# Optimization experiments

Hardware: AMD Instinct MI355X
Metric: run time of the kernel (lower is better)

The kernel has to match this reference:

```python
import jax, jax.numpy as jnp
import numpy as np

B = 32768
PASSES = 4

# mask layout: (batch, digit, row, col), values in {0,1}

def _to_lines(m, d):
    """Reorder so the last axis enumerates the 9 cells of a line and axis -2 the 9 lines."""
    if d == 'h':
        return m                      # lines = rows, cells = cols
    if d == 'v':
        return jnp.swapaxes(m, 2, 3)  # lines = cols, cells = rows
    b = m.shape[0]                    # lines = 3x3 boxes
    return m.reshape(b, 9, 3, 3, 3, 3).transpose(0, 1, 2, 4, 3, 5).reshape(b, 9, 9, 9)

_from_lines = _to_lines  # all three reorderings are self-inverse


def filter_line(m, d):
    """SudokuFilterHVBox: remove a solved cell's digit from all other cells in its line."""
    l = _to_lines(m, d)
    cnt = l.sum(axis=1, keepdims=True)                 # candidates per cell
    solved = l * (cnt == 1).astype(l.dtype)            # one-hot solved cells
    other = solved.sum(axis=-1, keepdims=True) - solved  # same digit solved elsewhere in line
    out = l * (other == 0).astype(l.dtype)
    return _from_lines(out, d)


def unique_line(m, d):
    """SudokuUniqueHVBox (hidden single): if a digit fits only one cell in a line, fix it."""
    l = _to_lines(m, d)
    cnt_line = l.sum(axis=-1, keepdims=True)           # per-digit count in the line
    hidden = l * (cnt_line == 1).astype(l.dtype)       # lone placements
    has = hidden.sum(axis=1, keepdims=True) > 0        # cell hosts a hidden single
    out = jnp.where(has, hidden, l)
    return _from_lines(out, d)


def doubles_line(m, d):
    """SudokuDigitsDoubles (naked pair): two identical 2-candidate cells in a line
    eliminate those digits from the rest of the line."""
    l = _to_lines(m, d)                                # (B, d, line, cell)
    cnt = l.sum(axis=1, keepdims=True)
    pm = l * (cnt == 2).astype(l.dtype)                # patterns of 2-candidate cells
    dot = jnp.einsum('bdlc,bdle->blce', pm, pm)        # pattern overlap between cells
    eye = jnp.eye(9, dtype=l.dtype)
    match = (dot == 2).astype(l.dtype) * (1.0 - eye)   # identical pair at another cell
    pairflag = match.sum(-1) > 0                       # (B, line, cell) part of a naked pair
    pair_digit = pm * pairflag[:, None, :, :].astype(l.dtype)
    total_pd = pair_digit.sum(-1, keepdims=True)       # digit belongs to some pair in line
    remove = (total_pd > 0) & (pair_digit == 0)
    out = l * (1.0 - remove.astype(l.dtype))
    return _from_lines(out, d)


def pointing(m, d):
    """SudokuDigitsInOneLineAtBox: if a digit's box candidates lie in one row/col,
    remove that digit from the rest of the row/col outside the box."""
    b = m.shape[0]
    v = m.reshape(b, 9, 3, 3, 3, 3)                    # (B, d, br, ri, bc, ci)
    if d == 'h':
        pres = v.sum(axis=5) > 0                       # (B,d,br,ri,bc) digit in row of box
        nrows = pres.sum(axis=3, keepdims=True)
        point = pres & (nrows == 1)                    # confined to single row within box
        tot = point.sum(axis=4, keepdims=True)         # over bc
        rem = (tot - point) > 0                        # pointing from another box hits us
        out = v * (1.0 - rem[..., None].astype(v.dtype))
    else:
        pres = v.sum(axis=3) > 0                       # (B,d,br,bc,ci) digit in col of box
        ncols = pres.sum(axis=4, keepdims=True)
        point = pres & (ncols == 1)
        tot = point.sum(axis=2, keepdims=True)         # over br
        rem = (tot - point) > 0
        out = v * (1.0 - rem[:, :, :, None, :, :].astype(v.dtype))
    return out.reshape(b, 9, 9, 9)


def _forward_mask(mask):
    for _ in range(PASSES):
        mask = filter_line(mask, 'box')
        mask = pointing(mask, 'h')
        mask = pointing(mask, 'v')
        mask = unique_line(mask, 'h')
        mask = unique_line(mask, 'v')
        mask = unique_line(mask, 'box')
        mask = doubles_line(mask, 'v')   # original code instantiates doubles_h with 'v'
        mask = doubles_line(mask, 'v')
        mask = doubles_line(mask, 'box')
    return mask


def setup_inputs() -> dict:
    key = jax.random.key(0)
    mask = jax.random.randint(key, (B, 9, 9, 9), 0, 2).astype(jnp.float32)
    return {"mask": mask}


def reference(mask):
    out = _forward_mask(mask)
    cnt = out.sum(axis=1)                              # candidates per cell
    solved = jnp.all(cnt == 1, axis=(1, 2))            # (B,) puzzle fully determined
    return (out, solved)
```

## Files before the change

kernel.cpp:

```cpp
#include <hip/hip_runtime.h>
#include <stdint.h>

#define NB 32768
#define NPASS 4
#define FULL27 0x07FFFFFFu
#define NBF (NB * 729)
#define NWORDS (NBF / 32)
#define PACK_BLKS (NWORDS / 256)
#define PUZ_PER_BLK 64
#define SOLVE_BLKS (NB / PUZ_PER_BLK)
#define BLK_DW 1458


__device__ __forceinline__ uint32_t colfold(uint32_t w) {
    return (w | (w >> 9) | (w >> 18)) & 0x1FFu;
}
__device__ __forceinline__ uint32_t colmaj2(uint32_t w) {
    return ((w & (w >> 9)) | ((w | (w >> 9)) & (w >> 18))) & 0x1FFu;
}
__device__ __forceinline__ uint32_t rotA(uint32_t v) {
    return (uint32_t)__builtin_amdgcn_update_dpp(0, (int)v, 0x09, 0xF, 0xF, true);
}
__device__ __forceinline__ uint32_t rotB(uint32_t v) {
    return (uint32_t)__builtin_amdgcn_update_dpp(0, (int)v, 0x12, 0xF, 0xF, true);
}

__global__ __launch_bounds__(256)
void pack_kernel(const uint32_t* __restrict__ in, uint32_t* __restrict__ ws) {
    const int g = blockIdx.x * 256 + threadIdx.x;
    const uint4* src = (const uint4*)in + (size_t)g * 8;
    uint32_t acc = 0u;
    #pragma unroll
    for (int j = 0; j < 8; ++j) {
        uint4 v = src[j];
        uint32_t n = ((v.x >> 23) & 1u) | (((v.y >> 23) & 1u) << 1)
                   | (((v.z >> 23) & 1u) << 2) | (((v.w >> 23) & 1u) << 3);
        acc |= n << (4 * j);
    }
    ws[g] = acc;
}

__global__ __launch_bounds__(256)
void solve_kernel(const uint32_t* __restrict__ ws, float* __restrict__ out,
                  float* __restrict__ solved) {
    __shared__ uint32_t lds[BLK_DW + 2];
    const int tid = threadIdx.x;
    const int q = tid >> 2;
    const int band = tid & 3;
    const int P0 = blockIdx.x * PUZ_PER_BLK;

    {
        const uint2* wsrc = (const uint2*)(ws + (size_t)blockIdx.x * BLK_DW);
        uint2* ldst = (uint2*)lds;
        #pragma unroll
        for (int i = 0; i < 3; ++i) {
            int j = i * 256 + tid;
            if (j < 729) ldst[j] = wsrc[j];
        }
    }
    __syncthreads();

    uint32_t bd[9];
    {
        const int bb0 = q * 729 + band * 27;
        #pragma unroll
        for (int d = 0; d < 9; ++d) {
            int bit = bb0 + d * 81;
            int di = bit >> 5, sh = bit & 31;
            uint64_t both = (uint64_t)lds[di] | ((uint64_t)lds[di + 1] << 32);
            bd[d] = (uint32_t)(both >> sh) & FULL27;
        }
    }
    __syncthreads();

    #pragma unroll 1
    for (int pass = 0; pass < NPASS; ++pass) {
        {
            uint32_t on = 0, tw = 0, fo = 0;
            #pragma unroll
            for (int d = 0; d < 9; ++d) {
                uint32_t c = on & bd[d];
                on ^= bd[d]; fo |= tw & c; tw ^= c;
            }
            uint32_t ex1 = on & ~tw & ~fo;
            #pragma unroll
            for (int d = 0; d < 9; ++d) {
                uint32_t s = bd[d] & ex1;
                #pragma unroll
                for (int k = 0; k < 3; ++k) {
                    uint32_t bm = 0x1C0E07u << (3 * k);
                    uint32_t sm = s & bm;
                    uint32_t multi = sm & (sm - 1u);
                    uint32_t keep = (sm == 0u) ? 0xFFFFFFFFu : (~bm | (multi ? 0u : sm));
                    bd[d] &= keep;
                }
            }
        }

        #pragma unroll
        for (int d = 0; d < 9; ++d) {
            uint32_t w = bd[d];
            uint32_t t = (w | (w >> 1) | (w >> 2)) & 0x01249249u;
            uint32_t sum = (t & 0x1FFu) + ((t >> 9) & 0x1FFu) + ((t >> 18) & 0x1FFu);
            uint32_t single = sum & ~(sum >> 1) & 0x49u;
            uint32_t point = t & (single * 0x40201u);
            uint32_t clearm = 0;
            #pragma unroll
            for (int r = 0; r < 3; ++r) {
                uint32_t pr = (point >> (9 * r)) & 0x1FFu;
                uint32_t multi = pr & (pr - 1u);
                uint32_t segkeep = multi ? 0u : pr * 7u;
                uint32_t rc = pr ? ((0x1FFu & ~segkeep) << (9 * r)) : 0u;
                clearm |= rc;
            }
            bd[d] = w & ~clearm;
        }

        {
            uint32_t pnt[9];
            #pragma unroll
            for (int d = 0; d < 9; ++d) {
                uint32_t w = bd[d];
                uint32_t qq = colfold(w);
                uint32_t u = (qq & 0x49u) + ((qq >> 1) & 0x49u) + ((qq >> 2) & 0x49u);
                uint32_t single = u & ~(u >> 1) & 0x49u;
                pnt[d] = qq & (single * 7u);
            }
            #pragma unroll
            for (int d = 0; d < 9; ++d) {
                uint32_t o = rotA(pnt[d]) | rotB(pnt[d]);
                bd[d] &= ~(o * 0x40201u);
            }
        }

        {
            uint32_t hid[9], has = 0;
            #pragma unroll
            for (int d = 0; d < 9; ++d) {
                uint32_t w = bd[d], h = 0;
                #pragma unroll
                for (int r = 0; r < 3; ++r) {
                    uint32_t x = w & (0x1FFu << (9 * r));
                    h |= (x & (x - 1u)) ? 0u : x;
                }
                hid[d] = h; has |= h;
            }
            #pragma unroll
            for (int d = 0; d < 9; ++d) bd[d] = (bd[d] & ~has) | hid[d];
        }

        {
            uint32_t hid[9], has = 0;
            #pragma unroll
            for (int d = 0; d < 9; ++d) {
                uint32_t w = bd[d];
                uint32_t q0 = colfold(w), m0 = colmaj2(w);
                uint32_t ex = q0 | (m0 << 9);
                uint32_t ea = rotA(ex);
                uint32_t eb = rotB(ex);
                uint32_t qa = ea & 0x1FFu, ma = ea >> 9;
                uint32_t qb = eb & 0x1FFu, mb = eb >> 9;
                uint32_t ge2 = m0 | ma | mb | (q0 & qa) | (q0 & qb) | (qa & qb);
                uint32_t ex1c = (q0 | qa | qb) & ~ge2;
                hid[d] = w & ((ex1c & q0) * 0x40201u);
                has |= hid[d];
            }
            #pragma unroll
            for (int d = 0; d < 9; ++d) bd[d] = (bd[d] & ~has) | hid[d];
        }

        {
            uint32_t hid[9], has = 0;
            #pragma unroll
            for (int d = 0; d < 9; ++d) {
                uint32_t w = bd[d], h = 0;
                #pragma unroll
                for (int k = 0; k < 3; ++k) {
                    uint32_t x = w & (0x1C0E07u << (3 * k));
                    h |= (x & (x - 1u)) ? 0u : x;
                }
                hid[d] = h; has |= h;
            }
            #pragma unroll
            for (int d = 0; d < 9; ++d) bd[d] = (bd[d] & ~has) | hid[d];
        }

        #pragma unroll 1
        for (int rep = 0; rep < 2; ++rep) {
            uint32_t on = 0, tw = 0, fo = 0;
            #pragma unroll
            for (int d = 0; d < 9; ++d) {
                uint32_t c = on & bd[d];
                on ^= bd[d]; fo |= tw & c; tw ^= c;
            }
            uint32_t ex2 = tw & ~on & ~fo;
            uint32_t Q[9], K[9];
            #pragma unroll
            for (int d = 0; d < 9; ++d) { Q[d] = bd[d] & ex2; K[d] = 0u; }
            #pragma unroll
            for (int d1 = 0; d1 < 9; ++d1)
                #pragma unroll
                for (int d2 = d1 + 1; d2 < 9; ++d2) {
                    uint32_t P = Q[d1] & Q[d2];
                    uint32_t f0 = colfold(P), g0 = colmaj2(P);
                    uint32_t ex = f0 | (g0 << 9);
                    uint32_t ea = rotA(ex);
                    uint32_t eb = rotB(ex);
                    uint32_t fa = ea & 0x1FFu, ga = ea >> 9;
                    uint32_t fb = eb & 0x1FFu, gb = eb >> 9;
                    uint32_t dup = g0 | ga | gb | (f0 & fa) | (f0 & fb) | (fa & fb);
                    uint32_t sK = P & (dup * 0x40201u);
                    K[d1] |= sK; K[d2] |= sK;
                }
            #pragma unroll
            for (int d = 0; d < 9; ++d) {
                uint32_t kc = colfold(K[d]);
                uint32_t cols = kc | rotA(kc) | rotB(kc);
                uint32_t em = cols * 0x40201u;
                bd[d] = (bd[d] & ~em) | K[d];
            }
        }

        {
            uint32_t on = 0, tw = 0, fo = 0;
            #pragma unroll
            for (int d = 0; d < 9; ++d) {
                uint32_t c = on & bd[d];
                on ^= bd[d]; fo |= tw & c; tw ^= c;
            }
            uint32_t ex2 = tw & ~on & ~fo;
            uint32_t Q[9], K[9];
            #pragma unroll
            for (int d = 0; d < 9; ++d) { Q[d] = bd[d] & ex2; K[d] = 0u; }
            #pragma unroll
            for (int d1 = 0; d1 < 9; ++d1)
                #pragma unroll
                for (int d2 = d1 + 1; d2 < 9; ++d2) {
                    uint32_t P = Q[d1] & Q[d2];
                    #pragma unroll
                    for (int k = 0; k < 3; ++k) {
                        uint32_t m = P & (0x1C0E07u << (3 * k));
                        uint32_t s = (m & (m - 1u)) ? m : 0u;
                        K[d1] |= s; K[d2] |= s;
                    }
                }
            #pragma unroll
            for (int d = 0; d < 9; ++d)
                #pragma unroll
                for (int k = 0; k < 3; ++k) {
                    uint32_t bm = 0x1C0E07u << (3 * k);
                    uint32_t t = K[d] & bm;
                    uint32_t mask = t ? (~bm | t) : 0xFFFFFFFFu;
                    bd[d] &= mask;
                }
        }
    }

    {
        uint32_t on = 0, tw = 0, fo = 0;
        #pragma unroll
        for (int d = 0; d < 9; ++d) {
            uint32_t c = on & bd[d];
            on ^= bd[d]; fo |= tw & c; tw ^= c;
        }
        uint32_t okb = ((on & ~tw & ~fo) == FULL27) ? 1u : 0u;
        uint32_t all = okb & rotA(okb) & rotB(okb);
        if (band == 0) solved[P0 + q] = all ? 1.0f : 0.0f;
    }

    for (int j = tid; j < BLK_DW + 2; j += 256) lds[j] = 0u;
    __syncthreads();
    if (band != 3) {
        const int pbit = q * 729;
        #pragma unroll
        for (int d = 0; d < 9; ++d) {
            int bitbase = pbit + d * 81 + band * 27;
            int di = bitbase >> 5;
            int sh = bitbase & 31;
            uint64_t both = (uint64_t)bd[d] << sh;
            atomicOr(&lds[di], (uint32_t)both);
            atomicOr(&lds[di + 1], (uint32_t)(both >> 32));
        }
    }
    __syncthreads();
    {
        float4* dst4 = (float4*)(out + (size_t)P0 * 729);
        #pragma unroll 4
        for (int i = 0; i < 46; ++i) {
            int j = i * 256 + tid;
            if (j < 11664) {
                uint32_t nib = (lds[j >> 3] >> ((j & 7) * 4)) & 0xFu;
                dst4[j] = make_float4((float)(nib & 1u), (float)((nib >> 1) & 1u),
                                      (float)((nib >> 2) & 1u), (float)((nib >> 3) & 1u));
            }
        }
    }
}

extern "C" void kernel_launch(void* const* d_in, const int* in_sizes, int n_in,
                              void* d_out, int out_size, void* d_ws, size_t ws_size,
                              hipStream_t stream) {
    const uint32_t* in = (const uint32_t*)d_in[0];
    float* out = (float*)d_out;
    float* solved = out + (size_t)NB * 729;
    uint32_t* ws = (uint32_t*)d_ws;

    pack_kernel<<<PACK_BLKS, 256, 0, stream>>>(in, ws);
    solve_kernel<<<SOLVE_BLKS, 256, 0, stream>>>(ws, out, solved);
}
```

Measured before the change: 216.2 us.

## Fuse bit-packing into solve kernel using DPP lane combining into LDS

Removes the separate pack kernel and its workspace round trip. Each solve block now reads its own float input slice directly, extracts one bit per float, and combines nibbles across neighbouring lanes with DPP swizzles before writing 16-bit halves into shared memory. This drops one launch and the global write and re-read of the packed workspace. In exchange, the solve kernel gets more load-phase work, clamped redundant loads, and lower per-block occupancy during the pack phase.

Measured after the change: 215.6 us. About the same (-0.3%).

```diff
diff --git a/kernel.cpp b/kernel.cpp
--- a/kernel.cpp
+++ b/kernel.cpp
@@ -4,12 +4,10 @@
 #define NB 32768
 #define NPASS 4
 #define FULL27 0x07FFFFFFu
-#define NBF (NB * 729)
-#define NWORDS (NBF / 32)
-#define PACK_BLKS (NWORDS / 256)
 #define PUZ_PER_BLK 64
 #define SOLVE_BLKS (NB / PUZ_PER_BLK)
 #define BLK_DW 1458
+#define BLK_V4 11664
 
 
 __device__ __forceinline__ uint32_t colfold(uint32_t w) {
@@ -24,38 +22,47 @@
 __device__ __forceinline__ uint32_t rotB(uint32_t v) {
     return (uint32_t)__builtin_amdgcn_update_dpp(0, (int)v, 0x12, 0xF, 0xF, true);
 }
+__device__ __forceinline__ uint32_t dppx1(uint32_t v) {
+    return (uint32_t)__builtin_amdgcn_update_dpp(0, (int)v, 0xB1, 0xF, 0xF, true);
+}
+__device__ __forceinline__ uint32_t dppx2(uint32_t v) {
+    return (uint32_t)__builtin_amdgcn_update_dpp(0, (int)v, 0x4E, 0xF, 0xF, true);
+}
 
 __global__ __launch_bounds__(256)
-void pack_kernel(const uint32_t* __restrict__ in, uint32_t* __restrict__ ws) {
-    const int g = blockIdx.x * 256 + threadIdx.x;
-    const uint4* src = (const uint4*)in + (size_t)g * 8;
-    uint32_t acc = 0u;
-    #pragma unroll
-    for (int j = 0; j < 8; ++j) {
-        uint4 v = src[j];
-        uint32_t n = ((v.x >> 23) & 1u) | (((v.y >> 23) & 1u) << 1)
-                   | (((v.z >> 23) & 1u) << 2) | (((v.w >> 23) & 1u) << 3);
-        acc |= n << (4 * j);
-    }
-    ws[g] = acc;
-}
-
-__global__ __launch_bounds__(256)
-void solve_kernel(const uint32_t* __restrict__ ws, float* __restrict__ out,
-                  float* __restrict__ solved) {
-    __shared__ uint32_t lds[BLK_DW + 2];
+void sudoku_kernel(const uint32_t* __restrict__ in, float* __restrict__ out,
+                   float* __restrict__ solved) {
+    __shared__ uint32_t pool[BLK_DW + 2];
     const int tid = threadIdx.x;
     const int q = tid >> 2;
     const int band = tid & 3;
     const int P0 = blockIdx.x * PUZ_PER_BLK;
 
     {
-        const uint2* wsrc = (const uint2*)(ws + (size_t)blockIdx.x * BLK_DW);
-        uint2* ldst = (uint2*)lds;
-        #pragma unroll
-        for (int i = 0; i < 3; ++i) {
-            int j = i * 256 + tid;
-            if (j < 729) ldst[j] = wsrc[j];
+        const uint4* src = (const uint4*)in + (size_t)blockIdx.x * BLK_V4;
+        uint16_t* hp = (uint16_t*)pool;
+        #pragma unroll 1
+        for (int ii = 0; ii < 6; ++ii) {
+            uint4 v[8];
+            #pragma unroll
+            for (int j = 0; j < 8; ++j) {
+                int vi = (ii * 8 + j) * 256 + tid;
+                if (vi > BLK_V4 - 1) vi = BLK_V4 - 1;
+                v[j] = src[vi];
+            }
+            #pragma unroll
+            for (int j = 0; j < 8; ++j) {
+                int it = ii * 8 + j;
+                uint32_t n = ((v[j].x >> 23) & 1u) | ((v[j].y >> 22) & 2u)
+                           | ((v[j].z >> 21) & 4u) | ((v[j].w >> 20) & 8u);
+                uint32_t b = n | (dppx1(n) << 4);
+                uint32_t h = b | (dppx2(b) << 8);
+                if ((tid & 3) == 0) {
+                    int D = it * 32 + (tid >> 3);
+                    if (D < BLK_DW)
+                        hp[2 * D + ((tid >> 2) & 1)] = (uint16_t)h;
+                }
+            }
         }
     }
     __syncthreads();
@@ -67,7 +74,7 @@
         for (int d = 0; d < 9; ++d) {
             int bit = bb0 + d * 81;
             int di = bit >> 5, sh = bit & 31;
-            uint64_t both = (uint64_t)lds[di] | ((uint64_t)lds[di + 1] << 32);
+            uint64_t both = (uint64_t)pool[di] | ((uint64_t)pool[di + 1] << 32);
             bd[d] = (uint32_t)(both >> sh) & FULL27;
         }
     }
@@ -268,7 +275,7 @@
         if (band == 0) solved[P0 + q] = all ? 1.0f : 0.0f;
     }
 
-    for (int j = tid; j < BLK_DW + 2; j += 256) lds[j] = 0u;
+    for (int j = tid; j < BLK_DW + 2; j += 256) pool[j] = 0u;
     __syncthreads();
     if (band != 3) {
         const int pbit = q * 729;
@@ -278,8 +285,8 @@
             int di = bitbase >> 5;
             int sh = bitbase & 31;
             uint64_t both = (uint64_t)bd[d] << sh;
-            atomicOr(&lds[di], (uint32_t)both);
-            atomicOr(&lds[di + 1], (uint32_t)(both >> 32));
+            atomicOr(&pool[di], (uint32_t)both);
+            atomicOr(&pool[di + 1], (uint32_t)(both >> 32));
         }
     }
     __syncthreads();
@@ -289,7 +296,7 @@
         for (int i = 0; i < 46; ++i) {
             int j = i * 256 + tid;
             if (j < 11664) {
-                uint32_t nib = (lds[j >> 3] >> ((j & 7) * 4)) & 0xFu;
+                uint32_t nib = (pool[j >> 3] >> ((j & 7) * 4)) & 0xFu;
                 dst4[j] = make_float4((float)(nib & 1u), (float)((nib >> 1) & 1u),
                                       (float)((nib >> 2) & 1u), (float)((nib >> 3) & 1u));
             }
@@ -303,8 +310,5 @@
     const uint32_t* in = (const uint32_t*)d_in[0];
     float* out = (float*)d_out;
     float* solved = out + (size_t)NB * 729;
-    uint32_t* ws = (uint32_t*)d_ws;
-
-    pack_kernel<<<PACK_BLKS, 256, 0, stream>>>(in, ws);
-    solve_kernel<<<SOLVE_BLKS, 256, 0, stream>>>(ws, out, solved);
-}
+    sudoku_kernel<<<SOLVE_BLKS, 256, 0, stream>>>(in, out, solved);
+}
```
